# Performance work log

Measured on AMD Instinct MI355X. Metric: run time of the kernel, lower is better.

Reference implementation:

```python
import jax, jax.numpy as jnp
import numpy as np

N_RAYS = 32768
HID = 64
MARCH_ITERS = 64
EPS = 1e-4
NEAR = 0.0
FAR = 1.0
T_FAR = 1.0
TPUT_B = 64
JITTER = 1.0 / TPUT_B  # fixed stand-in for random.random() * (2 / batch_size)


def _init_linear(key, fan_in, fan_out):
    kw, kb = jax.random.split(key)
    lim = 1.0 / np.sqrt(fan_in)
    W = jax.random.uniform(kw, (fan_in, fan_out), jnp.float32, -lim, lim)
    b = jax.random.uniform(kb, (fan_out,), jnp.float32, -lim, lim)
    return W, b


def setup_inputs() -> dict:
    key = jax.random.key(0)
    ks = jax.random.split(key, 6)
    rays = jax.random.normal(ks[0], (N_RAYS, 6), jnp.float32)
    W0, b0 = _init_linear(ks[1], 3, HID)
    W1, b1 = _init_linear(ks[2], HID, HID)
    W2, b2 = _init_linear(ks[3], HID, 1)
    Wr0, br0 = _init_linear(ks[4], 6, HID)
    Wr1, br1 = _init_linear(ks[5], HID, 3)
    return dict(rays=rays, W0=W0, b0=b0, W1=W1, b1=b1, W2=W2, b2=b2,
                Wr0=Wr0, br0=br0, Wr1=Wr1, br1=br1)


def _sdf(p, W0, b0, W1, b1, W2, b2):
    # p: [N, 3] -> signed distance [N, 1]
    h = jax.nn.relu(p @ W0 + b0)
    h = jax.nn.relu(h @ W1 + b1)
    return h @ W2 + b2


def _refl(p, d, Wr0, br0, Wr1, br1):
    # p, d: [N, 3] -> RGB [N, 3]
    h = jax.nn.relu(jnp.concatenate([p, d], axis=-1) @ Wr0 + br0)
    return jax.nn.sigmoid(h @ Wr1 + br1)


def reference(rays, W0, b0, W1, b1, W2, b2, Wr0, br0, Wr1, br1):
    r_o, r_d = rays[..., :3], rays[..., 3:]
    sdf = lambda p: _sdf(p, W0, b0, W1, b1, W2, b2)

    # --- sphere march (64 fixed iterations; early-exit break is a no-op
    # once all rays hit, since hit rays stop updating) ---
    hits0 = jnp.zeros(r_o.shape[:-1] + (1,), jnp.bool_)
    dist0 = jnp.full(r_o.shape[:-1] + (1,), NEAR, jnp.float32)

    def march(carry, _):
        hits, cd = carry
        d = sdf(r_o + r_d * cd)  # [N, 1]
        hits = hits | ((d < EPS) & (cd >= NEAR) & (cd <= FAR))
        cd = jnp.where(~hits, cd + d, cd)
        return (hits, cd), None

    (hit, t), _ = jax.lax.scan(march, (hits0, dist0), None, length=MARCH_ITERS)
    pts = r_o + r_d * t

    rgb = _refl(pts, r_d, Wr0, br0, Wr1, br1)
    rgb = jnp.where(hit, rgb, 0.0)  # out[~hit] = 0

    # --- throughput (index search under no_grad in the original) ---
    max_t = T_FAR + JITTER
    step = max_t / TPUT_B
    sg = jax.lax.stop_gradient
    sdf_ng = lambda p: _sdf(p, sg(W0), sg(b0), sg(W1), sg(b1), sg(W2), sg(b2))
    r_o_ng, r_d_ng = sg(r_o), sg(r_d)

    curr_min0 = sdf_ng(r_o_ng)[..., 0]          # [N]
    idxs0 = jnp.zeros_like(curr_min0, jnp.int32)

    def tloop(carry, i):
        cm, idxs = carry
        t_i = step * (i + 1).astype(jnp.float32)
        sd = sdf_ng(r_o_ng + t_i * r_d_ng)[..., 0]
        idxs = jnp.where(sd < cm, i + 1, idxs)
        return (jnp.minimum(cm, sd), idxs), None

    (_, idxs), _ = jax.lax.scan(tloop, (curr_min0, idxs0),
                                jnp.arange(TPUT_B, dtype=jnp.int32))

    best_pos = r_o + idxs[..., None].astype(jnp.float32) * step * r_d  # [N, 3]
    tput = sdf(best_pos)  # [N, 1], differentiable (outside no_grad in torch)

    return jnp.concatenate([rgb, tput], axis=-1)  # [N, 4]
```

## Files before the change

### kernel.cpp

```cpp
#include <hip/hip_runtime.h>
#include <math.h>

#define NRAYS        32768
#define MARCH_ITERS  64
#define EPS_         1e-4f
#define STEP_        ((1.0f + 1.0f/64.0f) / 64.0f)

typedef __attribute__((ext_vector_type(8)))  short    short8;
typedef __attribute__((ext_vector_type(4)))  float    float4v;
typedef __attribute__((ext_vector_type(4)))  unsigned uint4v;

__device__ __forceinline__ short8 mk_frag(unsigned p0, unsigned p1,
                                          unsigned p2, unsigned p3) {
    uint4v v = {p0, p1, p2, p3};
    return __builtin_bit_cast(short8, v);
}

__device__ __forceinline__ unsigned packbf(unsigned a, unsigned b) {
    return __builtin_amdgcn_perm(b, a, 0x07060302u);
}

struct Split3 { unsigned h, m, l; };
__device__ __forceinline__ Split3 split3(float x) {
    unsigned xu = __float_as_uint(x);
    float xh = __uint_as_float(xu & 0xFFFF0000u);
    float r  = x - xh;
    unsigned ru = __float_as_uint(r);
    float xm = __uint_as_float(ru & 0xFFFF0000u);
    float r2 = r - xm;
    return { xu, ru, __float_as_uint(r2) };
}

struct Split2 { unsigned h, r; };
__device__ __forceinline__ Split2 split2(float x) {
    unsigned xu = __float_as_uint(x);
    float xh = __uint_as_float(xu & 0xFFFF0000u);
    float rr = x - xh;
    return { xu, __float_as_uint(rr) };
}

__global__ __launch_bounds__(256, 2) void sdf_p5_k(
    const float* __restrict__ rays,
    const float* __restrict__ W0,  const float* __restrict__ b0,
    const float* __restrict__ W1,  const float* __restrict__ b1,
    const float* __restrict__ W2,  const float* __restrict__ b2,
    const float* __restrict__ Wr0, const float* __restrict__ br0,
    const float* __restrict__ Wr1, const float* __restrict__ br1,
    float* __restrict__ out)
{
    const int lane   = threadIdx.x & 63;
    const int waveId = threadIdx.x >> 6;
    const int quad   = lane >> 4;
    const int m      = lane & 15;
    const int rayBase = (blockIdx.x * 4 + waveId) * 16;

    const float* rp = rays + (rayBase + m) * 6;
    const float ox = rp[0], oy = rp[1], oz = rp[2];
    const float dx = rp[3], dy = rp[4], dz = rp[5];

    short8 A2[2][2][4];
    #pragma unroll
    for (int h = 0; h < 2; ++h)
        #pragma unroll
        for (int t = 0; t < 4; ++t) {
            unsigned ph[4], pm[4];
            #pragma unroll
            for (int jp = 0; jp < 4; ++jp) {
                int k0 = 32 * h + quad * 8 + 2 * jp;
                int j2 = 16 * t + m;
                Split2 a = split2(W1[k0 * 64 + j2]);
                Split2 b = split2(W1[(k0 + 1) * 64 + j2]);
                ph[jp] = packbf(a.h, b.h);
                pm[jp] = packbf(a.r, b.r);
            }
            A2[0][h][t] = mk_frag(ph[0], ph[1], ph[2], ph[3]);
            A2[1][h][t] = mk_frag(pm[0], pm[1], pm[2], pm[3]);
        }

    short8 A1[4];
    {
        const float* wbase = (quad == 0) ? W0 : (quad == 1) ? (W0 + 64)
                           : (quad == 2) ? (W0 + 128) : b0;
        #pragma unroll
        for (int t = 0; t < 4; ++t) {
            int j = 32 * (t >> 1) + 8 * (m >> 2) + 4 * (t & 1) + (m & 3);
            Split3 s = split3(wbase[j]);
            unsigned hh = packbf(s.h, s.h);
            unsigned hm = packbf(s.h, s.m);
            unsigned ml = packbf(s.m, s.l);
            unsigned l0 = packbf(s.l, 0u);
            bool is3 = (quad == 3);
            A1[t] = mk_frag(is3 ? hm : hh, is3 ? l0 : hm, is3 ? 0u : ml, 0u);
        }
    }

    float4v b1v[4], w2v[4];
    #pragma unroll
    for (int t = 0; t < 4; ++t) {
        int base = 16 * t + 4 * quad;
        b1v[t] = (float4v){b1[base], b1[base + 1], b1[base + 2], b1[base + 3]};
        w2v[t] = (float4v){W2[base], W2[base + 1], W2[base + 2], W2[base + 3]};
    }
    const float b2s = b2[0];
    const float4v z4 = {0.f, 0.f, 0.f, 0.f};

    auto buildB1 = [&](float px, float py, float pz) -> short8 {
        float c = (quad == 0) ? px : (quad == 1) ? py : pz;
        Split3 s = split3(c);
        unsigned d0 = packbf(s.h, s.m);
        unsigned d1 = packbf(s.l, s.h);
        unsigned d2 = packbf(s.m, s.h);
        if (quad == 3) { d0 = 0x3F803F80u; d1 = 0x00003F80u; d2 = 0u; }
        return mk_frag(d0, d1, d2, 0u);
    };

    auto tputFront = [&](float tt, short8* BH, short8* BM) {
        short8 B1t = buildB1(fmaf(dx, tt, ox), fmaf(dy, tt, oy), fmaf(dz, tt, oz));
        float4v C1t[4];
        #pragma unroll
        for (int t = 0; t < 4; ++t)
            C1t[t] = __builtin_amdgcn_mfma_f32_16x16x32_bf16(A1[t], B1t, z4, 0, 0, 0);
        unsigned PH[4][2], PM[4][2];
        #pragma unroll
        for (int t = 0; t < 4; ++t) {
            float v0 = fmaxf(C1t[t][0], 0.f), v1 = fmaxf(C1t[t][1], 0.f);
            float v2 = fmaxf(C1t[t][2], 0.f), v3 = fmaxf(C1t[t][3], 0.f);
            unsigned u0 = __float_as_uint(v0), u1 = __float_as_uint(v1);
            unsigned u2 = __float_as_uint(v2), u3 = __float_as_uint(v3);
            PH[t][0] = packbf(u0, u1); PH[t][1] = packbf(u2, u3);
            float r0 = v0 - __uint_as_float(u0 & 0xFFFF0000u);
            float r1 = v1 - __uint_as_float(u1 & 0xFFFF0000u);
            float r2 = v2 - __uint_as_float(u2 & 0xFFFF0000u);
            float r3 = v3 - __uint_as_float(u3 & 0xFFFF0000u);
            PM[t][0] = packbf(__float_as_uint(r0), __float_as_uint(r1));
            PM[t][1] = packbf(__float_as_uint(r2), __float_as_uint(r3));
        }
        #pragma unroll
        for (int h = 0; h < 2; ++h) {
            BH[h] = mk_frag(PH[2 * h][0], PH[2 * h][1],
                            PH[2 * h + 1][0], PH[2 * h + 1][1]);
            BM[h] = mk_frag(PM[2 * h][0], PM[2 * h][1],
                            PM[2 * h + 1][0], PM[2 * h + 1][1]);
        }
    };

    auto l3 = [&](const float4v* C2) -> float {
        float q0 = 0.f, q1 = 0.f, q2 = 0.f, q3 = 0.f;
        #pragma unroll
        for (int t = 0; t < 4; ++t) {
            q0 = fmaf(fmaxf(C2[t][0], 0.f), w2v[t][0], q0);
            q1 = fmaf(fmaxf(C2[t][1], 0.f), w2v[t][1], q1);
            q2 = fmaf(fmaxf(C2[t][2], 0.f), w2v[t][2], q2);
            q3 = fmaf(fmaxf(C2[t][3], 0.f), w2v[t][3], q3);
        }
        float part = (q0 + q1) + (q2 + q3);
        part += __shfl_xor(part, 16, 64);
        part += __shfl_xor(part, 32, 64);
        return b2s + part;
    };

    auto tputL2 = [&](const short8* BH, const short8* BM, float4v* C2t) {
        #pragma unroll
        for (int t = 0; t < 4; ++t) C2t[t] = b1v[t];
        #pragma unroll
        for (int h = 0; h < 2; ++h)
            #pragma unroll
            for (int t = 0; t < 4; ++t)
                C2t[t] = __builtin_amdgcn_mfma_f32_16x16x32_bf16(
                    A2[1][h][t], BH[h], C2t[t], 0, 0, 0);
        #pragma unroll
        for (int h = 0; h < 2; ++h)
            #pragma unroll
            for (int t = 0; t < 4; ++t)
                C2t[t] = __builtin_amdgcn_mfma_f32_16x16x32_bf16(
                    A2[0][h][t], BM[h], C2t[t], 0, 0, 0);
        #pragma unroll
        for (int h = 0; h < 2; ++h)
            #pragma unroll
            for (int t = 0; t < 4; ++t)
                C2t[t] = __builtin_amdgcn_mfma_f32_16x16x32_bf16(
                    A2[0][h][t], BH[h], C2t[t], 0, 0, 0);
    };

    const int pw_[5] = {1, 0, 1, 0, 0};
    const int ph_[5] = {1, 2, 0, 1, 0};

    bool  hit = false;
    float cd  = 0.f;
    float cm  = 0.f;

    short8 BtH[2], BtM[2];
    tputFront(STEP_, BtH, BtM);

    if (waveId & 1) {
        __builtin_amdgcn_s_sleep(7);
        __builtin_amdgcn_s_sleep(7);
        __builtin_amdgcn_s_sleep(7);
    }

    #pragma unroll 1
    for (int it = 0; it < MARCH_ITERS; ++it) {
        const bool doMarch = !__all((int)hit);
        float dt;
        short8 BnH[2], BnM[2];
        if (doMarch) {
            short8 B1m = buildB1(fmaf(dx, cd, ox), fmaf(dy, cd, oy), fmaf(dz, cd, oz));
            float4v C1m[4];
            #pragma unroll
            for (int t = 0; t < 4; ++t)
                C1m[t] = __builtin_amdgcn_mfma_f32_16x16x32_bf16(A1[t], B1m, z4, 0, 0, 0);
            unsigned P[3][4][2];
            #pragma unroll
            for (int t = 0; t < 4; ++t) {
                Split3 s0 = split3(fmaxf(C1m[t][0], 0.f));
                Split3 s1 = split3(fmaxf(C1m[t][1], 0.f));
                Split3 s2 = split3(fmaxf(C1m[t][2], 0.f));
                Split3 s3 = split3(fmaxf(C1m[t][3], 0.f));
                P[0][t][0] = packbf(s0.h, s1.h); P[0][t][1] = packbf(s2.h, s3.h);
                P[1][t][0] = packbf(s0.m, s1.m); P[1][t][1] = packbf(s2.m, s3.m);
                P[2][t][0] = packbf(s0.l, s1.l); P[2][t][1] = packbf(s2.l, s3.l);
            }
            short8 B2m[3][2];
            #pragma unroll
            for (int s = 0; s < 3; ++s)
                #pragma unroll
                for (int h = 0; h < 2; ++h)
                    B2m[s][h] = mk_frag(P[s][2 * h][0],     P[s][2 * h][1],
                                        P[s][2 * h + 1][0], P[s][2 * h + 1][1]);

            float4v C2m[4], C2t[4];
            #pragma unroll
            for (int t = 0; t < 4; ++t) { C2m[t] = b1v[t]; C2t[t] = b1v[t]; }
            #pragma unroll
            for (int p = 0; p < 5; ++p) {
                #pragma unroll
                for (int h = 0; h < 2; ++h)
                    #pragma unroll
                    for (int t = 0; t < 4; ++t)
                        C2m[t] = __builtin_amdgcn_mfma_f32_16x16x32_bf16(
                            A2[pw_[p]][h][t], B2m[ph_[p]][h], C2m[t], 0, 0, 0);
                if (p < 3) {
                    const short8* Bt = (p == 1) ? BtM : BtH;
                    const int sw = (p == 0) ? 1 : 0;
                    #pragma unroll
                    for (int h = 0; h < 2; ++h)
                        #pragma unroll
                        for (int t = 0; t < 4; ++t)
                            C2t[t] = __builtin_amdgcn_mfma_f32_16x16x32_bf16(
                                A2[sw][h][t], Bt[h], C2t[t], 0, 0, 0);
                }
            }
            tputFront(STEP_ * (float)(it + 2), BnH, BnM);
            float dm = l3(C2m);
            dt = l3(C2t);
            bool c = (dm < EPS_) && (cd >= 0.f) && (cd <= 1.f);
            hit = hit || c;
            if (!hit) cd += dm;
            if (it == 0) cm = dm;
        } else {
            float4v C2t[4];
            tputL2(BtH, BtM, C2t);
            tputFront(STEP_ * (float)(it + 2), BnH, BnM);
            dt = l3(C2t);
        }
        cm = fminf(cm, dt);
        #pragma unroll
        for (int h = 0; h < 2; ++h) { BtH[h] = BnH[h]; BtM[h] = BnM[h]; }
    }

    const float px = fmaf(dx, cd, ox), py = fmaf(dy, cd, oy), pz = fmaf(dz, cd, oz);
    float r0 = 0.f, r1 = 0.f, r2 = 0.f;
    #pragma unroll 4
    for (int jj = 0; jj < 16; ++jj) {
        int j = quad * 16 + jj;
        float a = fmaf(px, Wr0[j],
                  fmaf(py, Wr0[64 + j],
                  fmaf(pz, Wr0[128 + j],
                  fmaf(dx, Wr0[192 + j],
                  fmaf(dy, Wr0[256 + j],
                  fmaf(dz, Wr0[320 + j], br0[j]))))));
        a = fmaxf(a, 0.f);
        r0 = fmaf(a, Wr1[j * 3 + 0], r0);
        r1 = fmaf(a, Wr1[j * 3 + 1], r1);
        r2 = fmaf(a, Wr1[j * 3 + 2], r2);
    }
    r0 += __shfl_xor(r0, 16, 64); r0 += __shfl_xor(r0, 32, 64);
    r1 += __shfl_xor(r1, 16, 64); r1 += __shfl_xor(r1, 32, 64);
    r2 += __shfl_xor(r2, 16, 64); r2 += __shfl_xor(r2, 32, 64);
    r0 = 1.f / (1.f + expf(-(r0 + br1[0])));
    r1 = 1.f / (1.f + expf(-(r1 + br1[1])));
    r2 = 1.f / (1.f + expf(-(r2 + br1[2])));
    if (!hit) { r0 = 0.f; r1 = 0.f; r2 = 0.f; }

    if (lane < 16)
        reinterpret_cast<float4*>(out)[rayBase + lane] = make_float4(r0, r1, r2, cm);
}

extern "C" void kernel_launch(void* const* d_in, const int* in_sizes, int n_in,
                              void* d_out, int out_size, void* d_ws, size_t ws_size,
                              hipStream_t stream) {
    const float* rays = (const float*)d_in[0];
    const float* W0   = (const float*)d_in[1];
    const float* b0   = (const float*)d_in[2];
    const float* W1   = (const float*)d_in[3];
    const float* b1   = (const float*)d_in[4];
    const float* W2   = (const float*)d_in[5];
    const float* b2   = (const float*)d_in[6];
    const float* Wr0  = (const float*)d_in[7];
    const float* br0  = (const float*)d_in[8];
    const float* Wr1  = (const float*)d_in[9];
    const float* br1  = (const float*)d_in[10];
    float* out = (float*)d_out;

    hipLaunchKernelGGL(sdf_p5_k, dim3(NRAYS / 64), dim3(256), 0, stream,
                       rays, W0, b0, W1, b1, W2, b2, Wr0, br0, Wr1, br1, out);
}
```

Measured before the change: 201.5 us.

## Split march and throughput search into separate waves per 16-ray block

Each block now has two waves covering the same 16 rays. One wave runs the sphere march and reflectance, the other runs the 65-step throughput min-search. Before, a single wave interleaved both, and that fused schedule is removed. The march layer-2 now uses a 3-term bf16 split instead of 5 terms, and the throughput layer-2 drops the low-high term, both trading accuracy for fewer MFMAs. The march loop also breaks early once all rays hit. In exchange this launches twice as many waves and replaces the vector store with scalar stores.

```diff
diff --git a/kernel.cpp b/kernel.cpp
--- a/kernel.cpp
+++ b/kernel.cpp
@@ -39,7 +39,7 @@
     return { xu, __float_as_uint(rr) };
 }
 
-__global__ __launch_bounds__(256, 2) void sdf_p5_k(
+__global__ __launch_bounds__(128, 3) void sdf_mt_k(
     const float* __restrict__ rays,
     const float* __restrict__ W0,  const float* __restrict__ b0,
     const float* __restrict__ W1,  const float* __restrict__ b1,
@@ -48,17 +48,17 @@
     const float* __restrict__ Wr1, const float* __restrict__ br1,
     float* __restrict__ out)
 {
-    const int lane   = threadIdx.x & 63;
-    const int waveId = threadIdx.x >> 6;
-    const int quad   = lane >> 4;
-    const int m      = lane & 15;
-    const int rayBase = (blockIdx.x * 4 + waveId) * 16;
+    const int lane = threadIdx.x & 63;
+    const int kind = threadIdx.x >> 6;
+    const int quad = lane >> 4;
+    const int m    = lane & 15;
+    const int rayBase = blockIdx.x * 16;
 
     const float* rp = rays + (rayBase + m) * 6;
     const float ox = rp[0], oy = rp[1], oz = rp[2];
     const float dx = rp[3], dy = rp[4], dz = rp[5];
 
-    short8 A2[2][2][4];
+    short8 A2h[2][4], A2m[2][4];
     #pragma unroll
     for (int h = 0; h < 2; ++h)
         #pragma unroll
@@ -73,8 +73,8 @@
                 ph[jp] = packbf(a.h, b.h);
                 pm[jp] = packbf(a.r, b.r);
             }
-            A2[0][h][t] = mk_frag(ph[0], ph[1], ph[2], ph[3]);
-            A2[1][h][t] = mk_frag(pm[0], pm[1], pm[2], pm[3]);
+            A2h[h][t] = mk_frag(ph[0], ph[1], ph[2], ph[3]);
+            A2m[h][t] = mk_frag(pm[0], pm[1], pm[2], pm[3]);
         }
 
     short8 A1[4];
@@ -114,17 +114,17 @@
         return mk_frag(d0, d1, d2, 0u);
     };
 
-    auto tputFront = [&](float tt, short8* BH, short8* BM) {
-        short8 B1t = buildB1(fmaf(dx, tt, ox), fmaf(dy, tt, oy), fmaf(dz, tt, oz));
-        float4v C1t[4];
+    auto front = [&](float px, float py, float pz, short8* BH, short8* BM) {
+        short8 B1 = buildB1(px, py, pz);
+        float4v C1[4];
         #pragma unroll
         for (int t = 0; t < 4; ++t)
-            C1t[t] = __builtin_amdgcn_mfma_f32_16x16x32_bf16(A1[t], B1t, z4, 0, 0, 0);
+            C1[t] = __builtin_amdgcn_mfma_f32_16x16x32_bf16(A1[t], B1, z4, 0, 0, 0);
         unsigned PH[4][2], PM[4][2];
         #pragma unroll
         for (int t = 0; t < 4; ++t) {
-            float v0 = fmaxf(C1t[t][0], 0.f), v1 = fmaxf(C1t[t][1], 0.f);
-            float v2 = fmaxf(C1t[t][2], 0.f), v3 = fmaxf(C1t[t][3], 0.f);
+            float v0 = fmaxf(C1[t][0], 0.f), v1 = fmaxf(C1[t][1], 0.f);
+            float v2 = fmaxf(C1[t][2], 0.f), v3 = fmaxf(C1[t][3], 0.f);
             unsigned u0 = __float_as_uint(v0), u1 = __float_as_uint(v1);
             unsigned u2 = __float_as_uint(v2), u3 = __float_as_uint(v3);
             PH[t][0] = packbf(u0, u1); PH[t][1] = packbf(u2, u3);
@@ -159,141 +159,99 @@
         return b2s + part;
     };
 
-    auto tputL2 = [&](const short8* BH, const short8* BM, float4v* C2t) {
-        #pragma unroll
-        for (int t = 0; t < 4; ++t) C2t[t] = b1v[t];
-        #pragma unroll
-        for (int h = 0; h < 2; ++h)
-            #pragma unroll
-            for (int t = 0; t < 4; ++t)
-                C2t[t] = __builtin_amdgcn_mfma_f32_16x16x32_bf16(
-                    A2[1][h][t], BH[h], C2t[t], 0, 0, 0);
-        #pragma unroll
-        for (int h = 0; h < 2; ++h)
-            #pragma unroll
-            for (int t = 0; t < 4; ++t)
-                C2t[t] = __builtin_amdgcn_mfma_f32_16x16x32_bf16(
-                    A2[0][h][t], BM[h], C2t[t], 0, 0, 0);
-        #pragma unroll
-        for (int h = 0; h < 2; ++h)
-            #pragma unroll
-            for (int t = 0; t < 4; ++t)
-                C2t[t] = __builtin_amdgcn_mfma_f32_16x16x32_bf16(
-                    A2[0][h][t], BH[h], C2t[t], 0, 0, 0);
-    };
-
-    const int pw_[5] = {1, 0, 1, 0, 0};
-    const int ph_[5] = {1, 2, 0, 1, 0};
-
-    bool  hit = false;
-    float cd  = 0.f;
-    float cm  = 0.f;
-
-    short8 BtH[2], BtM[2];
-    tputFront(STEP_, BtH, BtM);
-
-    if (waveId & 1) {
-        __builtin_amdgcn_s_sleep(7);
-        __builtin_amdgcn_s_sleep(7);
-        __builtin_amdgcn_s_sleep(7);
-    }
-
-    #pragma unroll 1
-    for (int it = 0; it < MARCH_ITERS; ++it) {
-        const bool doMarch = !__all((int)hit);
-        float dt;
-        short8 BnH[2], BnM[2];
-        if (doMarch) {
-            short8 B1m = buildB1(fmaf(dx, cd, ox), fmaf(dy, cd, oy), fmaf(dz, cd, oz));
-            float4v C1m[4];
-            #pragma unroll
-            for (int t = 0; t < 4; ++t)
-                C1m[t] = __builtin_amdgcn_mfma_f32_16x16x32_bf16(A1[t], B1m, z4, 0, 0, 0);
-            unsigned P[3][4][2];
-            #pragma unroll
-            for (int t = 0; t < 4; ++t) {
-                Split3 s0 = split3(fmaxf(C1m[t][0], 0.f));
-                Split3 s1 = split3(fmaxf(C1m[t][1], 0.f));
-                Split3 s2 = split3(fmaxf(C1m[t][2], 0.f));
-                Split3 s3 = split3(fmaxf(C1m[t][3], 0.f));
-                P[0][t][0] = packbf(s0.h, s1.h); P[0][t][1] = packbf(s2.h, s3.h);
-                P[1][t][0] = packbf(s0.m, s1.m); P[1][t][1] = packbf(s2.m, s3.m);
-                P[2][t][0] = packbf(s0.l, s1.l); P[2][t][1] = packbf(s2.l, s3.l);
-            }
-            short8 B2m[3][2];
-            #pragma unroll
-            for (int s = 0; s < 3; ++s)
-                #pragma unroll
-                for (int h = 0; h < 2; ++h)
-                    B2m[s][h] = mk_frag(P[s][2 * h][0],     P[s][2 * h][1],
-                                        P[s][2 * h + 1][0], P[s][2 * h + 1][1]);
-
-            float4v C2m[4], C2t[4];
-            #pragma unroll
-            for (int t = 0; t < 4; ++t) { C2m[t] = b1v[t]; C2t[t] = b1v[t]; }
-            #pragma unroll
-            for (int p = 0; p < 5; ++p) {
-                #pragma unroll
-                for (int h = 0; h < 2; ++h)
-                    #pragma unroll
-                    for (int t = 0; t < 4; ++t)
-                        C2m[t] = __builtin_amdgcn_mfma_f32_16x16x32_bf16(
-                            A2[pw_[p]][h][t], B2m[ph_[p]][h], C2m[t], 0, 0, 0);
-                if (p < 3) {
-                    const short8* Bt = (p == 1) ? BtM : BtH;
-                    const int sw = (p == 0) ? 1 : 0;
-                    #pragma unroll
-                    for (int h = 0; h < 2; ++h)
-                        #pragma unroll
-                        for (int t = 0; t < 4; ++t)
-                            C2t[t] = __builtin_amdgcn_mfma_f32_16x16x32_bf16(
-                                A2[sw][h][t], Bt[h], C2t[t], 0, 0, 0);
-                }
-            }
-            tputFront(STEP_ * (float)(it + 2), BnH, BnM);
-            float dm = l3(C2m);
-            dt = l3(C2t);
+    if (kind == 0) {
+        bool  hit = false;
+        float cd  = 0.f;
+        #pragma unroll 1
+        for (int it = 0; it < MARCH_ITERS; ++it) {
+            if (__all(hit)) break;
+            short8 BH[2], BM[2];
+            front(fmaf(dx, cd, ox), fmaf(dy, cd, oy), fmaf(dz, cd, oz), BH, BM);
+            float4v C2[4];
+            #pragma unroll
+            for (int t = 0; t < 4; ++t) C2[t] = b1v[t];
+            #pragma unroll
+            for (int h = 0; h < 2; ++h)
+                #pragma unroll
+                for (int t = 0; t < 4; ++t)
+                    C2[t] = __builtin_amdgcn_mfma_f32_16x16x32_bf16(
+                        A2m[h][t], BH[h], C2[t], 0, 0, 0);
+            #pragma unroll
+            for (int h = 0; h < 2; ++h)
+                #pragma unroll
+                for (int t = 0; t < 4; ++t)
+                    C2[t] = __builtin_amdgcn_mfma_f32_16x16x32_bf16(
+                        A2h[h][t], BM[h], C2[t], 0, 0, 0);
+            #pragma unroll
+            for (int h = 0; h < 2; ++h)
+                #pragma unroll
+                for (int t = 0; t < 4; ++t)
+                    C2[t] = __builtin_amdgcn_mfma_f32_16x16x32_bf16(
+                        A2h[h][t], BH[h], C2[t], 0, 0, 0);
+            float dm = l3(C2);
             bool c = (dm < EPS_) && (cd >= 0.f) && (cd <= 1.f);
             hit = hit || c;
             if (!hit) cd += dm;
-            if (it == 0) cm = dm;
-        } else {
-            float4v C2t[4];
-            tputL2(BtH, BtM, C2t);
-            tputFront(STEP_ * (float)(it + 2), BnH, BnM);
-            dt = l3(C2t);
-        }
-        cm = fminf(cm, dt);
-        #pragma unroll
-        for (int h = 0; h < 2; ++h) { BtH[h] = BnH[h]; BtM[h] = BnM[h]; }
+        }
+
+        const float px = fmaf(dx, cd, ox), py = fmaf(dy, cd, oy), pz = fmaf(dz, cd, oz);
+        float r0 = 0.f, r1 = 0.f, r2 = 0.f;
+        #pragma unroll 4
+        for (int jj = 0; jj < 16; ++jj) {
+            int j = quad * 16 + jj;
+            float a = fmaf(px, Wr0[j],
+                      fmaf(py, Wr0[64 + j],
+                      fmaf(pz, Wr0[128 + j],
+                      fmaf(dx, Wr0[192 + j],
+                      fmaf(dy, Wr0[256 + j],
+                      fmaf(dz, Wr0[320 + j], br0[j]))))));
+            a = fmaxf(a, 0.f);
+            r0 = fmaf(a, Wr1[j * 3 + 0], r0);
+            r1 = fmaf(a, Wr1[j * 3 + 1], r1);
+            r2 = fmaf(a, Wr1[j * 3 + 2], r2);
+        }
+        r0 += __shfl_xor(r0, 16, 64); r0 += __shfl_xor(r0, 32, 64);
+        r1 += __shfl_xor(r1, 16, 64); r1 += __shfl_xor(r1, 32, 64);
+        r2 += __shfl_xor(r2, 16, 64); r2 += __shfl_xor(r2, 32, 64);
+        r0 = 1.f / (1.f + expf(-(r0 + br1[0])));
+        r1 = 1.f / (1.f + expf(-(r1 + br1[1])));
+        r2 = 1.f / (1.f + expf(-(r2 + br1[2])));
+        if (!hit) { r0 = 0.f; r1 = 0.f; r2 = 0.f; }
+        if (lane < 16) {
+            float* op = out + (rayBase + lane) * 4;
+            op[0] = r0; op[1] = r1; op[2] = r2;
+        }
+    } else {
+        short8 BH[2], BM[2], BnH[2], BnM[2];
+        front(ox, oy, oz, BH, BM);
+        float cm = 3.4e38f;
+        #pragma unroll 2
+        for (int i = 0; i <= 64; ++i) {
+            float4v C2[4];
+            #pragma unroll
+            for (int t = 0; t < 4; ++t) C2[t] = b1v[t];
+            #pragma unroll
+            for (int h = 0; h < 2; ++h)
+                #pragma unroll
+                for (int t = 0; t < 4; ++t)
+                    C2[t] = __builtin_amdgcn_mfma_f32_16x16x32_bf16(
+                        A2h[h][t], BM[h], C2[t], 0, 0, 0);
+            #pragma unroll
+            for (int h = 0; h < 2; ++h)
+                #pragma unroll
+                for (int t = 0; t < 4; ++t)
+                    C2[t] = __builtin_amdgcn_mfma_f32_16x16x32_bf16(
+                        A2h[h][t], BH[h], C2[t], 0, 0, 0);
+            float tn = STEP_ * (float)(i + 1);
+            front(fmaf(dx, tn, ox), fmaf(dy, tn, oy), fmaf(dz, tn, oz), BnH, BnM);
+            float dt = l3(C2);
+            cm = fminf(cm, dt);
+            #pragma unroll
+            for (int h = 0; h < 2; ++h) { BH[h] = BnH[h]; BM[h] = BnM[h]; }
+        }
+        if (lane < 16)
+            out[(rayBase + lane) * 4 + 3] = cm;
     }
-
-    const float px = fmaf(dx, cd, ox), py = fmaf(dy, cd, oy), pz = fmaf(dz, cd, oz);
-    float r0 = 0.f, r1 = 0.f, r2 = 0.f;
-    #pragma unroll 4
-    for (int jj = 0; jj < 16; ++jj) {
-        int j = quad * 16 + jj;
-        float a = fmaf(px, Wr0[j],
-                  fmaf(py, Wr0[64 + j],
-                  fmaf(pz, Wr0[128 + j],
-                  fmaf(dx, Wr0[192 + j],
-                  fmaf(dy, Wr0[256 + j],
-                  fmaf(dz, Wr0[320 + j], br0[j]))))));
-        a = fmaxf(a, 0.f);
-        r0 = fmaf(a, Wr1[j * 3 + 0], r0);
-        r1 = fmaf(a, Wr1[j * 3 + 1], r1);
-        r2 = fmaf(a, Wr1[j * 3 + 2], r2);
-    }
-    r0 += __shfl_xor(r0, 16, 64); r0 += __shfl_xor(r0, 32, 64);
-    r1 += __shfl_xor(r1, 16, 64); r1 += __shfl_xor(r1, 32, 64);
-    r2 += __shfl_xor(r2, 16, 64); r2 += __shfl_xor(r2, 32, 64);
-    r0 = 1.f / (1.f + expf(-(r0 + br1[0])));
-    r1 = 1.f / (1.f + expf(-(r1 + br1[1])));
-    r2 = 1.f / (1.f + expf(-(r2 + br1[2])));
-    if (!hit) { r0 = 0.f; r1 = 0.f; r2 = 0.f; }
-
-    if (lane < 16)
-        reinterpret_cast<float4*>(out)[rayBase + lane] = make_float4(r0, r1, r2, cm);
 }
 
 extern "C" void kernel_launch(void* const* d_in, const int* in_sizes, int n_in,
@@ -312,6 +270,6 @@
     const float* br1  = (const float*)d_in[10];
     float* out = (float*)d_out;
 
-    hipLaunchKernelGGL(sdf_p5_k, dim3(NRAYS / 64), dim3(256), 0, stream,
+    hipLaunchKernelGGL(sdf_mt_k, dim3(NRAYS / 16), dim3(128), 0, stream,
                        rays, W0, b0, W1, b1, W2, b2, Wr0, br0, Wr1, br1, out);
 }
```

New measurement: 188.0 us. 1.07x faster.
